# Optimization experiments

Measured on AMD Instinct MI355X. Metric: run time of the kernel, lower is better.

Reference implementation:

```python
import math
import jax, jax.numpy as jnp
import numpy as np

B, N, D = 32, 1025, 768        # batch, tokens (incl. CLS), backbone channels
C, CD, TD = 64, 128, 256       # num_clusters, cluster_dim, token_dim
REG = 0.1
SINKHORN_ITERS = 5


def setup_inputs() -> dict:
    key = jax.random.key(0)
    ks = jax.random.split(key, 9)
    inv = 1.0 / math.sqrt(D)
    return {
        "x": jax.random.normal(ks[0], (B, N, D), dtype=jnp.float32),
        "Wf": jax.random.normal(ks[1], (D, CD), dtype=jnp.float32) * inv,
        "bf": jnp.zeros((CD,), dtype=jnp.float32),
        "Ws": jax.random.normal(ks[2], (D, C), dtype=jnp.float32) * inv,
        "bs": jnp.zeros((C,), dtype=jnp.float32),
        "Wt": jax.random.normal(ks[3], (D, TD), dtype=jnp.float32) * inv,
        "bt": jnp.zeros((TD,), dtype=jnp.float32),
        "anchors": jax.random.normal(ks[4], (C, CD), dtype=jnp.float32) * 0.1,
        "dust_bin": jnp.array(1.0, dtype=jnp.float32),
        "sharpness": jnp.array(5.0, dtype=jnp.float32),
    }


def _sinkhorn_log(log_a, log_b, M, num_iters, reg):
    # log-domain Sinkhorn: M [B, C+1, Nt], log_a [B, C+1], log_b [B, Nt]
    M = M / reg
    u = jnp.zeros_like(log_a)
    v = jnp.zeros_like(log_b)
    for _ in range(num_iters):
        u = log_a - jax.nn.logsumexp(M + v[:, None, :], axis=2)
        v = log_b - jax.nn.logsumexp(M + u[:, :, None], axis=1)
    return M + u[:, :, None] + v[:, None, :]


def reference(x, Wf, bf, Ws, bs, Wt, bt, anchors, dust_bin, sharpness):
    Bx, Nx, _ = x.shape
    n_tok = Nx - 1
    nC = anchors.shape[0]

    t_global = x[:, 0]            # [B, D]
    fi = x[:, 1:]                 # [B, Nt, D]

    f = fi @ Wf + bf              # [B, Nt, CD]
    s = jnp.einsum('bnd,dc->bcn', fi, Ws) + bs[None, :, None]  # [B, C, Nt]
    s = s * sharpness

    dust = jnp.broadcast_to(dust_bin, (Bx, 1, n_tok))
    s_aug = jnp.concatenate([s, dust], axis=1)  # [B, C+1, Nt]

    log_b = jnp.full((Bx, n_tok), -math.log(n_tok), dtype=x.dtype)
    # n_tok (1024) > nC (64): marginals with dustbin absorbing excess mass
    log_a = jnp.concatenate([
        jnp.full((Bx, nC), -math.log(n_tok), dtype=x.dtype),
        jnp.full((Bx, 1), math.log(n_tok - nC) - math.log(n_tok), dtype=x.dtype),
    ], axis=1)

    log_P = _sinkhorn_log(log_a, log_b, s_aug, SINKHORN_ITERS, REG)
    p = jnp.exp(log_P)[:, :-1, :]  # [B, C, Nt], drop dustbin row

    # sum_n p[b,c,n] * (2*f[b,n,d] - anchors[c,d])  == GEMM + rank-1 correction
    v_agg = 2.0 * jnp.einsum('bcn,bnd->bcd', p, f) \
            - p.sum(axis=2)[:, :, None] * anchors[None]  # [B, C, CD]

    v_local = v_agg.reshape(Bx, -1)   # [B, C*CD]
    v_global = t_global @ Wt + bt     # [B, TD]
    f_out = jnp.concatenate([v_global, v_local], axis=-1)
    norm = jnp.maximum(jnp.linalg.norm(f_out, axis=-1, keepdims=True), 1e-12)
    return f_out / norm
```

## Files before the change

### kernel.cpp

```cpp
#include <hip/hip_runtime.h>

typedef unsigned short u16;
typedef __attribute__((ext_vector_type(8))) short bf16x8;
typedef __attribute__((ext_vector_type(4))) float f32x4;
typedef __attribute__((ext_vector_type(4))) short s16x4;

#define OUTW 8448

static __device__ __forceinline__ float bf2f(u16 u) {
    union { unsigned int i; float f; } x; x.i = ((unsigned int)u) << 16; return x.f;
}
static __device__ __forceinline__ u16 f2bf(float f) {
    union { float f; unsigned int i; } x; x.f = f;
    unsigned int lsb = (x.i >> 16) & 1u;
    return (u16)((x.i + 0x7fffu + lsb) >> 16);
}

__global__ __launch_bounds__(256, 2) void k_gemm1(
    const float* __restrict__ x, const float* __restrict__ Wf, const float* __restrict__ bf_,
    const float* __restrict__ Ws, const float* __restrict__ bs_, const float* __restrict__ sharp,
    u16* __restrict__ fT, float* __restrict__ sM)
{
    __shared__ u16 Asm[128][72];
    __shared__ u16 Bsm[64][72];
    const int tid  = threadIdx.x;
    const int lane = tid & 63;
    const int w    = tid >> 6;
    const int bm = blockIdx.x, bn = blockIdx.y;
    const int b  = bm >> 3;
    const int n0 = (bm & 7) << 7;
    const float* Abase = x + ((size_t)b * 1025 + 1 + n0) * 768;
    const float* Bsrc; int bstride, coff;
    if (bn < 2) { Bsrc = Wf; bstride = 128; coff = bn * 64; }
    else        { Bsrc = Ws; bstride = 64;  coff = 0; }

    f32x4 acc[2][4] = {};
    const int arow = tid >> 4;
    const int acol = (tid & 15) << 2;
    const int bc   = tid & 63;
    const int bkg  = tid >> 6;

    for (int ks = 0; ks < 12; ++ks) {
        const int k0 = ks * 64;
        #pragma unroll
        for (int pp = 0; pp < 8; ++pp) {
            const int r = arow + pp * 16;
            const float4 v = *(const float4*)(Abase + (size_t)r * 768 + k0 + acol);
            u16* dA = &Asm[r][acol];
            dA[0] = f2bf(v.x); dA[1] = f2bf(v.y); dA[2] = f2bf(v.z); dA[3] = f2bf(v.w);
        }
        {
            u16 tmp[16];
            #pragma unroll
            for (int i = 0; i < 16; ++i)
                tmp[i] = f2bf(Bsrc[(size_t)(k0 + bkg * 16 + i) * bstride + coff + bc]);
            u16* dB = &Bsm[bc][bkg * 16];
            *(s16x4*)(dB)      = *(const s16x4*)(tmp);
            *(s16x4*)(dB + 4)  = *(const s16x4*)(tmp + 4);
            *(s16x4*)(dB + 8)  = *(const s16x4*)(tmp + 8);
            *(s16x4*)(dB + 12) = *(const s16x4*)(tmp + 12);
        }
        __syncthreads();
        #pragma unroll
        for (int kk = 0; kk < 2; ++kk) {
            const int kb = kk * 32 + ((lane >> 4) << 3);
            bf16x8 af[2], bfr[4];
            #pragma unroll
            for (int mt = 0; mt < 2; ++mt)
                af[mt] = *(const bf16x8*)&Asm[w * 32 + mt * 16 + (lane & 15)][kb];
            #pragma unroll
            for (int nt = 0; nt < 4; ++nt)
                bfr[nt] = *(const bf16x8*)&Bsm[nt * 16 + (lane & 15)][kb];
            #pragma unroll
            for (int mt = 0; mt < 2; ++mt)
                #pragma unroll
                for (int nt = 0; nt < 4; ++nt)
                    acc[mt][nt] = __builtin_amdgcn_mfma_f32_16x16x32_bf16(af[mt], bfr[nt], acc[mt][nt], 0, 0, 0);
        }
        __syncthreads();
    }
    const int rbase = (lane >> 4) << 2;
    const int cl = lane & 15;
    if (bn < 2) {
        #pragma unroll
        for (int mt = 0; mt < 2; ++mt) {
            const int nbase = n0 + w * 32 + mt * 16 + rbase;
            #pragma unroll
            for (int nt = 0; nt < 4; ++nt) {
                const int c = bn * 64 + nt * 16 + cl;
                const float bias = bf_[c];
                u16 pk[4];
                #pragma unroll
                for (int r = 0; r < 4; ++r) pk[r] = f2bf(acc[mt][nt][r] + bias);
                *(s16x4*)&fT[((size_t)b * 128 + c) * 1024 + nbase] = *(const s16x4*)pk;
            }
        }
    } else {
        const float sc = sharp[0] * 10.0f;
        #pragma unroll
        for (int mt = 0; mt < 2; ++mt) {
            const int nbase = n0 + w * 32 + mt * 16 + rbase;
            #pragma unroll
            for (int nt = 0; nt < 4; ++nt) {
                const int cm = nt * 16 + cl;
                const float bias = bs_[cm];
                float4 v;
                v.x = (acc[mt][nt][0] + bias) * sc;
                v.y = (acc[mt][nt][1] + bias) * sc;
                v.z = (acc[mt][nt][2] + bias) * sc;
                v.w = (acc[mt][nt][3] + bias) * sc;
                *(float4*)&sM[((size_t)b * 64 + cm) * 1024 + nbase] = v;
            }
        }
    }
}

__global__ __launch_bounds__(1024, 1) void k_sinkhorn(
    const float* __restrict__ sM, u16* __restrict__ p_out)
{
    __shared__ u16   Ksm[64][1024];
    __shared__ float beta[1024];
    __shared__ float alpha[65];
    const int b = blockIdx.x;
    const int tid = threadIdx.x;
    const int lane = tid & 63;
    const int w = tid >> 6;
    const float* Mb = sM + (size_t)b * 64 * 1024;

    #pragma unroll
    for (int i = 0; i < 4; ++i) {
        const int c = w + 16 * i;
        const float* row = Mb + (size_t)c * 1024;
        float vals[16]; float mx = -3.4e38f;
        #pragma unroll
        for (int j = 0; j < 16; ++j) { vals[j] = row[lane + 64 * j]; mx = fmaxf(mx, vals[j]); }
        #pragma unroll
        for (int off = 32; off > 0; off >>= 1) mx = fmaxf(mx, __shfl_xor(mx, off));
        #pragma unroll
        for (int j = 0; j < 16; ++j) Ksm[c][lane + 64 * j] = f2bf(__expf(vals[j] - mx));
    }
    beta[tid] = 1.0f;
    __syncthreads();

    const float a_c = 1.0f / 1024.0f, a_dust = 960.0f / 1024.0f, b_n = 1.0f / 1024.0f;
    for (int it = 0; it < 5; ++it) {
        #pragma unroll
        for (int i = 0; i < 4; ++i) {
            const int c = w + 16 * i;
            float s = 0.f;
            #pragma unroll
            for (int j = 0; j < 16; ++j)
                s += bf2f(Ksm[c][lane + 64 * j]) * beta[lane + 64 * j];
            #pragma unroll
            for (int off = 32; off > 0; off >>= 1) s += __shfl_xor(s, off);
            if (lane == 0) alpha[c] = a_c / s;
        }
        if (w == 0) {
            float s = 0.f;
            #pragma unroll
            for (int j = 0; j < 16; ++j) s += beta[lane + 64 * j];
            #pragma unroll
            for (int off = 32; off > 0; off >>= 1) s += __shfl_xor(s, off);
            if (lane == 0) alpha[64] = a_dust / s;
        }
        __syncthreads();
        float s = alpha[64];
        #pragma unroll 16
        for (int c = 0; c < 64; ++c) s += bf2f(Ksm[c][tid]) * alpha[c];
        beta[tid] = b_n / s;
        __syncthreads();
    }
    const float bnv = beta[tid];
    u16* pc = p_out + (size_t)b * 64 * 1024 + tid;
    #pragma unroll 8
    for (int c = 0; c < 64; ++c)
        pc[(size_t)c * 1024] = f2bf(alpha[c] * bf2f(Ksm[c][tid]) * bnv);
}

__global__ __launch_bounds__(1024, 1) void k_agg(
    const u16* __restrict__ p, const u16* __restrict__ fT,
    const float* __restrict__ anchors, float* __restrict__ out)
{
    __shared__ float ps[64];
    const int b = blockIdx.x;
    const int tid = threadIdx.x;
    const int lane = tid & 63;
    const int w = tid >> 6;
    {
        const int c = tid >> 4;
        const int j = tid & 15;
        const u16* pr = p + ((size_t)b * 64 + c) * 1024 + j * 64;
        float s = 0.f;
        #pragma unroll 16
        for (int i = 0; i < 64; ++i) s += bf2f(pr[i]);
        #pragma unroll
        for (int off = 8; off > 0; off >>= 1) s += __shfl_xor(s, off);
        if (j == 0) ps[c] = s;
    }
    __syncthreads();
    const int mt = w & 3;
    const int ng = w >> 2;
    const u16* arow  = p  + ((size_t)b * 64  + mt * 16 + (lane & 15)) * 1024 + ((lane >> 4) << 3);
    const u16* brow0 = fT + ((size_t)b * 128 + ng * 32 + (lane & 15)) * 1024 + ((lane >> 4) << 3);
    const u16* brow1 = brow0 + 16 * 1024;
    f32x4 acc[2] = {};
    for (int ks = 0; ks < 32; ++ks) {
        const int k0 = ks * 32;
        bf16x8 a  = *(const bf16x8*)(arow  + k0);
        bf16x8 b0 = *(const bf16x8*)(brow0 + k0);
        bf16x8 b1 = *(const bf16x8*)(brow1 + k0);
        acc[0] = __builtin_amdgcn_mfma_f32_16x16x32_bf16(a, b0, acc[0], 0, 0, 0);
        acc[1] = __builtin_amdgcn_mfma_f32_16x16x32_bf16(a, b1, acc[1], 0, 0, 0);
    }
    #pragma unroll
    for (int nt = 0; nt < 2; ++nt) {
        const int d = ng * 32 + nt * 16 + (lane & 15);
        #pragma unroll
        for (int r = 0; r < 4; ++r) {
            const int c = mt * 16 + ((lane >> 4) << 2) + r;
            out[(size_t)b * OUTW + 256 + c * 128 + d] = 2.0f * acc[nt][r] - ps[c] * anchors[c * 128 + d];
        }
    }
}

__global__ void k_vglobal(const float* __restrict__ x, const float* __restrict__ Wt,
                          float* __restrict__ vg)
{
    const int kc = blockIdx.x >> 5;
    const int b  = blockIdx.x & 31;
    const int d  = threadIdx.x;
    const float* xr = x  + (size_t)b * (1025 * 768) + kc * 96;
    const float* wp = Wt + (size_t)kc * 96 * 256 + d;
    float acc = 0.f;
    #pragma unroll 8
    for (int k = 0; k < 96; ++k) acc += xr[k] * wp[(size_t)k * 256];
    vg[(size_t)blockIdx.x * 256 + d] = acc;
}

__global__ __launch_bounds__(256) void k_norm(const float* __restrict__ vg, const float* __restrict__ bt,
                                              float* __restrict__ out)
{
    const int b = blockIdx.x;
    const int t = threadIdx.x;
    float vals[33];
    float ss = 0.f;
    {
        float v = bt[t];
        #pragma unroll
        for (int kc = 0; kc < 8; ++kc) v += vg[(size_t)(kc * 32 + b) * 256 + t];
        vals[0] = v; ss += v * v;
    }
    #pragma unroll
    for (int j = 1; j < 33; ++j) {
        const float v = out[(size_t)b * OUTW + j * 256 + t];
        vals[j] = v; ss += v * v;
    }
    #pragma unroll
    for (int off = 32; off > 0; off >>= 1) ss += __shfl_xor(ss, off);
    __shared__ float part[4];
    if ((t & 63) == 0) part[t >> 6] = ss;
    __syncthreads();
    const float tot = part[0] + part[1] + part[2] + part[3];
    const float inv = 1.0f / fmaxf(sqrtf(tot), 1e-12f);
    #pragma unroll
    for (int j = 0; j < 33; ++j)
        out[(size_t)b * OUTW + j * 256 + t] = vals[j] * inv;
}

extern "C" void kernel_launch(void* const* d_in, const int* in_sizes, int n_in,
                              void* d_out, int out_size, void* d_ws, size_t ws_size,
                              hipStream_t stream)
{
    const float* x      = (const float*)d_in[0];
    const float* Wf     = (const float*)d_in[1];
    const float* bf_    = (const float*)d_in[2];
    const float* Ws     = (const float*)d_in[3];
    const float* bs_    = (const float*)d_in[4];
    const float* Wt     = (const float*)d_in[5];
    const float* bt     = (const float*)d_in[6];
    const float* anchors= (const float*)d_in[7];
    const float* sharp  = (const float*)d_in[9];

    char* ws = (char*)d_ws;
    u16*   fT = (u16*)(ws);
    float* sM = (float*)(ws + 8388608);
    u16*   p  = (u16*)(ws + 16777216);
    float* vg = (float*)(ws + 20971520);
    float* out = (float*)d_out;

    k_gemm1   <<<dim3(256, 3), 256,  0, stream>>>(x, Wf, bf_, Ws, bs_, sharp, fT, sM);
    k_vglobal <<<dim3(256),    256,  0, stream>>>(x, Wt, vg);
    k_sinkhorn<<<dim3(32),     1024, 0, stream>>>(sM, p);
    k_agg     <<<dim3(32),     1024, 0, stream>>>(p, fT, anchors, out);
    k_norm    <<<dim3(32),     256,  0, stream>>>(vg, bt, out);
}
```

Measured before the change: 276.3 us.

## Fuse GEMM column tiles, prefetch loads, vectorize Sinkhorn, compute row sums in-kernel

The first GEMM now computes all 192 output columns (Wf and Ws) in one 512-thread block, so x is read and converted once instead of three times. It also register-prefetches the next K slice while MFMAs run. The Sinkhorn kernel uses vectorized shared-memory accesses with a new per-thread partition, and writes p row sums itself so the aggregation kernel no longer re-reads p to sum it. The costs are higher register pressure and fewer GEMM blocks (256), which may lower occupancy.

```diff
diff --git a/kernel.cpp b/kernel.cpp
--- a/kernel.cpp
+++ b/kernel.cpp
@@ -2,6 +2,7 @@
 
 typedef unsigned short u16;
 typedef __attribute__((ext_vector_type(8))) short bf16x8;
+typedef __attribute__((ext_vector_type(8))) short s16x8;
 typedef __attribute__((ext_vector_type(4))) float f32x4;
 typedef __attribute__((ext_vector_type(4))) short s16x4;
 
@@ -16,93 +17,115 @@
     return (u16)((x.i + 0x7fffu + lsb) >> 16);
 }
 
-__global__ __launch_bounds__(256, 2) void k_gemm1(
+__global__ __launch_bounds__(512, 2) void k_gemm1(
     const float* __restrict__ x, const float* __restrict__ Wf, const float* __restrict__ bf_,
     const float* __restrict__ Ws, const float* __restrict__ bs_, const float* __restrict__ sharp,
     u16* __restrict__ fT, float* __restrict__ sM)
 {
     __shared__ u16 Asm[128][72];
-    __shared__ u16 Bsm[64][72];
+    __shared__ u16 Bsm[192][72];
     const int tid  = threadIdx.x;
     const int lane = tid & 63;
     const int w    = tid >> 6;
-    const int bm = blockIdx.x, bn = blockIdx.y;
-    const int b  = bm >> 3;
-    const int n0 = (bm & 7) << 7;
+    const int b    = blockIdx.x >> 3;
+    const int n0   = (blockIdx.x & 7) << 7;
     const float* Abase = x + ((size_t)b * 1025 + 1 + n0) * 768;
-    const float* Bsrc; int bstride, coff;
-    if (bn < 2) { Bsrc = Wf; bstride = 128; coff = bn * 64; }
-    else        { Bsrc = Ws; bstride = 64;  coff = 0; }
-
-    f32x4 acc[2][4] = {};
-    const int arow = tid >> 4;
-    const int acol = (tid & 15) << 2;
-    const int bc   = tid & 63;
-    const int bkg  = tid >> 6;
+
+    const int arow = tid >> 2;
+    const int ac0  = (tid & 3) << 4;
+    int   bkg[3]; const float* bptr[3]; int bstr[3]; int bcol[3];
+    #pragma unroll
+    for (int s = 0; s < 3; ++s) {
+        const int idx = tid + s * 512;
+        const int kg  = idx / 192;
+        const int col = idx - kg * 192;
+        bkg[s] = kg; bcol[s] = col;
+        if (col < 128) { bptr[s] = Wf + col; bstr[s] = 128; }
+        else           { bptr[s] = Ws + (col - 128); bstr[s] = 64; }
+    }
+
+    f32x4 acc[4][3] = {};
+    const int wm = w >> 2, wn = w & 3;
+    const int wr = wm * 64, wc = wn * 48;
+
+    float4 pa[4];
+    float  pb[3][8];
+
+    #pragma unroll
+    for (int q = 0; q < 4; ++q)
+        pa[q] = *(const float4*)(Abase + (size_t)arow * 768 + ac0 + q * 4);
+    #pragma unroll
+    for (int s = 0; s < 3; ++s)
+        #pragma unroll
+        for (int j = 0; j < 8; ++j)
+            pb[s][j] = bptr[s][(size_t)(bkg[s] * 8 + j) * bstr[s]];
 
     for (int ks = 0; ks < 12; ++ks) {
-        const int k0 = ks * 64;
-        #pragma unroll
-        for (int pp = 0; pp < 8; ++pp) {
-            const int r = arow + pp * 16;
-            const float4 v = *(const float4*)(Abase + (size_t)r * 768 + k0 + acol);
-            u16* dA = &Asm[r][acol];
-            dA[0] = f2bf(v.x); dA[1] = f2bf(v.y); dA[2] = f2bf(v.z); dA[3] = f2bf(v.w);
-        }
         {
-            u16 tmp[16];
-            #pragma unroll
-            for (int i = 0; i < 16; ++i)
-                tmp[i] = f2bf(Bsrc[(size_t)(k0 + bkg * 16 + i) * bstride + coff + bc]);
-            u16* dB = &Bsm[bc][bkg * 16];
-            *(s16x4*)(dB)      = *(const s16x4*)(tmp);
-            *(s16x4*)(dB + 4)  = *(const s16x4*)(tmp + 4);
-            *(s16x4*)(dB + 8)  = *(const s16x4*)(tmp + 8);
-            *(s16x4*)(dB + 12) = *(const s16x4*)(tmp + 12);
+            u16 ta[16];
+            #pragma unroll
+            for (int q = 0; q < 4; ++q) {
+                ta[q*4+0] = f2bf(pa[q].x); ta[q*4+1] = f2bf(pa[q].y);
+                ta[q*4+2] = f2bf(pa[q].z); ta[q*4+3] = f2bf(pa[q].w);
+            }
+            *(s16x8*)&Asm[arow][ac0]     = *(const s16x8*)(ta);
+            *(s16x8*)&Asm[arow][ac0 + 8] = *(const s16x8*)(ta + 8);
+            #pragma unroll
+            for (int s = 0; s < 3; ++s) {
+                u16 tb[8];
+                #pragma unroll
+                for (int j = 0; j < 8; ++j) tb[j] = f2bf(pb[s][j]);
+                *(s16x8*)&Bsm[bcol[s]][bkg[s] * 8] = *(const s16x8*)(tb);
+            }
         }
         __syncthreads();
+        if (ks < 11) {
+            const int k0 = (ks + 1) * 64;
+            #pragma unroll
+            for (int q = 0; q < 4; ++q)
+                pa[q] = *(const float4*)(Abase + (size_t)arow * 768 + k0 + ac0 + q * 4);
+            #pragma unroll
+            for (int s = 0; s < 3; ++s)
+                #pragma unroll
+                for (int j = 0; j < 8; ++j)
+                    pb[s][j] = bptr[s][(size_t)(k0 + bkg[s] * 8 + j) * bstr[s]];
+        }
         #pragma unroll
         for (int kk = 0; kk < 2; ++kk) {
             const int kb = kk * 32 + ((lane >> 4) << 3);
-            bf16x8 af[2], bfr[4];
-            #pragma unroll
-            for (int mt = 0; mt < 2; ++mt)
-                af[mt] = *(const bf16x8*)&Asm[w * 32 + mt * 16 + (lane & 15)][kb];
-            #pragma unroll
-            for (int nt = 0; nt < 4; ++nt)
-                bfr[nt] = *(const bf16x8*)&Bsm[nt * 16 + (lane & 15)][kb];
-            #pragma unroll
-            for (int mt = 0; mt < 2; ++mt)
-                #pragma unroll
-                for (int nt = 0; nt < 4; ++nt)
+            bf16x8 af[4], bfr[3];
+            #pragma unroll
+            for (int mt = 0; mt < 4; ++mt)
+                af[mt] = *(const bf16x8*)&Asm[wr + mt * 16 + (lane & 15)][kb];
+            #pragma unroll
+            for (int nt = 0; nt < 3; ++nt)
+                bfr[nt] = *(const bf16x8*)&Bsm[wc + nt * 16 + (lane & 15)][kb];
+            #pragma unroll
+            for (int mt = 0; mt < 4; ++mt)
+                #pragma unroll
+                for (int nt = 0; nt < 3; ++nt)
                     acc[mt][nt] = __builtin_amdgcn_mfma_f32_16x16x32_bf16(af[mt], bfr[nt], acc[mt][nt], 0, 0, 0);
         }
         __syncthreads();
     }
     const int rbase = (lane >> 4) << 2;
     const int cl = lane & 15;
-    if (bn < 2) {
-        #pragma unroll
-        for (int mt = 0; mt < 2; ++mt) {
-            const int nbase = n0 + w * 32 + mt * 16 + rbase;
-            #pragma unroll
-            for (int nt = 0; nt < 4; ++nt) {
-                const int c = bn * 64 + nt * 16 + cl;
+    const float sc = sharp[0] * 10.0f;
+    #pragma unroll
+    for (int mt = 0; mt < 4; ++mt) {
+        const int nbase = n0 + wr + mt * 16 + rbase;
+        #pragma unroll
+        for (int nt = 0; nt < 3; ++nt) {
+            const int col16 = wc + nt * 16;
+            const int c = col16 + cl;
+            if (col16 < 128) {
                 const float bias = bf_[c];
                 u16 pk[4];
                 #pragma unroll
                 for (int r = 0; r < 4; ++r) pk[r] = f2bf(acc[mt][nt][r] + bias);
                 *(s16x4*)&fT[((size_t)b * 128 + c) * 1024 + nbase] = *(const s16x4*)pk;
-            }
-        }
-    } else {
-        const float sc = sharp[0] * 10.0f;
-        #pragma unroll
-        for (int mt = 0; mt < 2; ++mt) {
-            const int nbase = n0 + w * 32 + mt * 16 + rbase;
-            #pragma unroll
-            for (int nt = 0; nt < 4; ++nt) {
-                const int cm = nt * 16 + cl;
+            } else {
+                const int cm = c - 128;
                 const float bias = bs_[cm];
                 float4 v;
                 v.x = (acc[mt][nt][0] + bias) * sc;
@@ -116,88 +139,138 @@
 }
 
 __global__ __launch_bounds__(1024, 1) void k_sinkhorn(
-    const float* __restrict__ sM, u16* __restrict__ p_out)
+    const float* __restrict__ sM, u16* __restrict__ p_out, float* __restrict__ rs_out)
 {
     __shared__ u16   Ksm[64][1024];
-    __shared__ float beta[1024];
-    __shared__ float alpha[65];
+    __shared__ float betas[1024];
+    __shared__ float alph[68];
+    const int b   = blockIdx.x;
+    const int tid = threadIdx.x;
+    const int l   = tid & 63;
+    const int w   = tid >> 6;
+    const float* Mb = sM + (size_t)b * 64 * 1024;
+
+    #pragma unroll
+    for (int i = 0; i < 4; ++i) {
+        const int c = w * 4 + i;
+        float v[16];
+        #pragma unroll
+        for (int q = 0; q < 4; ++q)
+            *(float4*)(v + q * 4) = *(const float4*)(Mb + (size_t)c * 1024 + l * 16 + q * 4);
+        float mx = v[0];
+        #pragma unroll
+        for (int j = 1; j < 16; ++j) mx = fmaxf(mx, v[j]);
+        #pragma unroll
+        for (int off = 32; off > 0; off >>= 1) mx = fmaxf(mx, __shfl_xor(mx, off));
+        u16 e[16];
+        #pragma unroll
+        for (int j = 0; j < 16; ++j) e[j] = f2bf(__expf(v[j] - mx));
+        *(s16x8*)&Ksm[c][l * 16]     = *(const s16x8*)(e);
+        *(s16x8*)&Ksm[c][l * 16 + 8] = *(const s16x8*)(e + 8);
+    }
+    betas[tid] = 1.0f;
+    __syncthreads();
+
+    const float a_c = 1.0f / 1024.0f, a_dust = 960.0f / 1024.0f, b_n = 1.0f / 1024.0f;
+    const int r8 = (l & 7) * 8;
+    const int cg = w * 8 + (l >> 3);
+    const int bwi = (cg & 63) + ((cg >> 6) << 9);
+
+    for (int it = 0; it < 5; ++it) {
+        float bb[16];
+        #pragma unroll
+        for (int j = 0; j < 2; ++j)
+            #pragma unroll
+            for (int m = 0; m < 8; ++m)
+                bb[j * 8 + m] = betas[l + m * 64 + j * 512];
+        float sb = 0.f;
+        #pragma unroll
+        for (int j = 0; j < 16; ++j) sb += bb[j];
+        #pragma unroll
+        for (int off = 32; off > 0; off >>= 1) sb += __shfl_xor(sb, off);
+        #pragma unroll
+        for (int i = 0; i < 4; ++i) {
+            const int c = w * 4 + i;
+            float s = 0.f;
+            #pragma unroll
+            for (int j = 0; j < 2; ++j) {
+                const bf16x8 kr = *(const bf16x8*)&Ksm[c][8 * l + 512 * j];
+                #pragma unroll
+                for (int m = 0; m < 8; ++m)
+                    s += bf2f((u16)kr[m]) * bb[j * 8 + m];
+            }
+            #pragma unroll
+            for (int off = 32; off > 0; off >>= 1) s += __shfl_xor(s, off);
+            if (l == 0) alph[c] = a_c / s;
+        }
+        if (tid == 0) alph[64] = a_dust / sb;
+        __syncthreads();
+        f32x4 a0 = *(const f32x4*)&alph[r8];
+        f32x4 a1 = *(const f32x4*)&alph[r8 + 4];
+        const float ad = alph[64];
+        float sc8[8] = {};
+        #pragma unroll
+        for (int i = 0; i < 8; ++i) {
+            const bf16x8 kb = *(const bf16x8*)&Ksm[r8 + i][cg * 8];
+            const float av = (i < 4) ? a0[i] : a1[i - 4];
+            #pragma unroll
+            for (int m = 0; m < 8; ++m)
+                sc8[m] += bf2f((u16)kb[m]) * av;
+        }
+        #pragma unroll
+        for (int off = 1; off < 8; off <<= 1)
+            #pragma unroll
+            for (int m = 0; m < 8; ++m)
+                sc8[m] += __shfl_xor(sc8[m], off);
+        if ((l & 7) == 0) {
+            #pragma unroll
+            for (int m = 0; m < 8; ++m)
+                betas[bwi + m * 64] = b_n / (sc8[m] + ad);
+        }
+        __syncthreads();
+    }
+
+    float bb[16];
+    #pragma unroll
+    for (int j = 0; j < 2; ++j)
+        #pragma unroll
+        for (int m = 0; m < 8; ++m)
+            bb[j * 8 + m] = betas[l + m * 64 + j * 512];
+    #pragma unroll
+    for (int i = 0; i < 4; ++i) {
+        const int c = w * 4 + i;
+        const float ac = alph[c];
+        float pv[16]; float s = 0.f;
+        #pragma unroll
+        for (int j = 0; j < 2; ++j) {
+            const bf16x8 kr = *(const bf16x8*)&Ksm[c][8 * l + 512 * j];
+            #pragma unroll
+            for (int m = 0; m < 8; ++m) {
+                const float t = bf2f((u16)kr[m]) * bb[j * 8 + m];
+                pv[j * 8 + m] = t; s += t;
+            }
+        }
+        #pragma unroll
+        for (int off = 32; off > 0; off >>= 1) s += __shfl_xor(s, off);
+        if (l == 0) rs_out[b * 64 + c] = ac * s;
+        u16 pk[16];
+        #pragma unroll
+        for (int j = 0; j < 16; ++j) pk[j] = f2bf(ac * pv[j]);
+        u16* pg = p_out + ((size_t)b * 64 + c) * 1024 + 8 * l;
+        *(s16x8*)(pg)       = *(const s16x8*)(pk);
+        *(s16x8*)(pg + 512) = *(const s16x8*)(pk + 8);
+    }
+}
+
+__global__ __launch_bounds__(1024, 1) void k_agg(
+    const u16* __restrict__ p, const u16* __restrict__ fT,
+    const float* __restrict__ rs, const float* __restrict__ anchors,
+    float* __restrict__ out)
+{
     const int b = blockIdx.x;
     const int tid = threadIdx.x;
     const int lane = tid & 63;
     const int w = tid >> 6;
-    const float* Mb = sM + (size_t)b * 64 * 1024;
-
-    #pragma unroll
-    for (int i = 0; i < 4; ++i) {
-        const int c = w + 16 * i;
-        const float* row = Mb + (size_t)c * 1024;
-        float vals[16]; float mx = -3.4e38f;
-        #pragma unroll
-        for (int j = 0; j < 16; ++j) { vals[j] = row[lane + 64 * j]; mx = fmaxf(mx, vals[j]); }
-        #pragma unroll
-        for (int off = 32; off > 0; off >>= 1) mx = fmaxf(mx, __shfl_xor(mx, off));
-        #pragma unroll
-        for (int j = 0; j < 16; ++j) Ksm[c][lane + 64 * j] = f2bf(__expf(vals[j] - mx));
-    }
-    beta[tid] = 1.0f;
-    __syncthreads();
-
-    const float a_c = 1.0f / 1024.0f, a_dust = 960.0f / 1024.0f, b_n = 1.0f / 1024.0f;
-    for (int it = 0; it < 5; ++it) {
-        #pragma unroll
-        for (int i = 0; i < 4; ++i) {
-            const int c = w + 16 * i;
-            float s = 0.f;
-            #pragma unroll
-            for (int j = 0; j < 16; ++j)
-                s += bf2f(Ksm[c][lane + 64 * j]) * beta[lane + 64 * j];
-            #pragma unroll
-            for (int off = 32; off > 0; off >>= 1) s += __shfl_xor(s, off);
-            if (lane == 0) alpha[c] = a_c / s;
-        }
-        if (w == 0) {
-            float s = 0.f;
-            #pragma unroll
-            for (int j = 0; j < 16; ++j) s += beta[lane + 64 * j];
-            #pragma unroll
-            for (int off = 32; off > 0; off >>= 1) s += __shfl_xor(s, off);
-            if (lane == 0) alpha[64] = a_dust / s;
-        }
-        __syncthreads();
-        float s = alpha[64];
-        #pragma unroll 16
-        for (int c = 0; c < 64; ++c) s += bf2f(Ksm[c][tid]) * alpha[c];
-        beta[tid] = b_n / s;
-        __syncthreads();
-    }
-    const float bnv = beta[tid];
-    u16* pc = p_out + (size_t)b * 64 * 1024 + tid;
-    #pragma unroll 8
-    for (int c = 0; c < 64; ++c)
-        pc[(size_t)c * 1024] = f2bf(alpha[c] * bf2f(Ksm[c][tid]) * bnv);
-}
-
-__global__ __launch_bounds__(1024, 1) void k_agg(
-    const u16* __restrict__ p, const u16* __restrict__ fT,
-    const float* __restrict__ anchors, float* __restrict__ out)
-{
-    __shared__ float ps[64];
-    const int b = blockIdx.x;
-    const int tid = threadIdx.x;
-    const int lane = tid & 63;
-    const int w = tid >> 6;
-    {
-        const int c = tid >> 4;
-        const int j = tid & 15;
-        const u16* pr = p + ((size_t)b * 64 + c) * 1024 + j * 64;
-        float s = 0.f;
-        #pragma unroll 16
-        for (int i = 0; i < 64; ++i) s += bf2f(pr[i]);
-        #pragma unroll
-        for (int off = 8; off > 0; off >>= 1) s += __shfl_xor(s, off);
-        if (j == 0) ps[c] = s;
-    }
-    __syncthreads();
     const int mt = w & 3;
     const int ng = w >> 2;
     const u16* arow  = p  + ((size_t)b * 64  + mt * 16 + (lane & 15)) * 1024 + ((lane >> 4) << 3);
@@ -218,7 +291,7 @@
         #pragma unroll
         for (int r = 0; r < 4; ++r) {
             const int c = mt * 16 + ((lane >> 4) << 2) + r;
-            out[(size_t)b * OUTW + 256 + c * 128 + d] = 2.0f * acc[nt][r] - ps[c] * anchors[c * 128 + d];
+            out[(size_t)b * OUTW + 256 + c * 128 + d] = 2.0f * acc[nt][r] - rs[b * 64 + c] * anchors[c * 128 + d];
         }
     }
 }
@@ -286,11 +359,12 @@
     float* sM = (float*)(ws + 8388608);
     u16*   p  = (u16*)(ws + 16777216);
     float* vg = (float*)(ws + 20971520);
+    float* rs = (float*)(ws + 21233664);
     float* out = (float*)d_out;
 
-    k_gemm1   <<<dim3(256, 3), 256,  0, stream>>>(x, Wf, bf_, Ws, bs_, sharp, fT, sM);
-    k_vglobal <<<dim3(256),    256,  0, stream>>>(x, Wt, vg);
-    k_sinkhorn<<<dim3(32),     1024, 0, stream>>>(sM, p);
-    k_agg     <<<dim3(32),     1024, 0, stream>>>(p, fT, anchors, out);
-    k_norm    <<<dim3(32),     256,  0, stream>>>(vg, bt, out);
-}
+    k_gemm1   <<<dim3(256), 512,  0, stream>>>(x, Wf, bf_, Ws, bs_, sharp, fT, sM);
+    k_vglobal <<<dim3(256), 256,  0, stream>>>(x, Wt, vg);
+    k_sinkhorn<<<dim3(32),  1024, 0, stream>>>(sM, p, rs);
+    k_agg     <<<dim3(32),  1024, 0, stream>>>(p, fT, rs, anchors, out);
+    k_norm    <<<dim3(32),  256,  0, stream>>>(vg, bt, out);
+}
```

After: 275.3 us. Within noise of the previous version (-0.4%).
